# Optimization experiments

Measured on AMD Instinct MI355X. Metric: run time of the kernel, lower is better.

The kernel has to match this reference:

```python
import jax, jax.numpy as jnp
import numpy as np

B, N, U, K = 2, 768, 64, 8
IN = 2 * U + K  # 136
SLOPE = 0.01    # torch LeakyReLU default


def setup_inputs() -> dict:
    key = jax.random.key(0)
    ks = jax.random.split(key, 12)
    seq_embed = jax.random.normal(ks[0], (B, N, U), dtype=jnp.float32)
    vals = jax.random.uniform(ks[1], (N, N, K), dtype=jnp.float32)
    edge = (jax.random.uniform(ks[2], (N, N)) < 0.05) | jnp.eye(N, dtype=bool)
    relational_encoding = vals * edge[:, :, None].astype(jnp.float32)
    s = 0.05
    inp = {"seq_embed": seq_embed, "relational_encoding": relational_encoding}
    # per-hop MLP params: hop k has Linear(IN,IN) then Linear(IN,1); W stored (in,out)
    inp["w1_1"] = jax.random.normal(ks[3], (IN, IN), dtype=jnp.float32) * s
    inp["b1_1"] = jax.random.normal(ks[4], (IN,), dtype=jnp.float32) * s
    inp["w1_2"] = jax.random.normal(ks[5], (IN, 1), dtype=jnp.float32) * s
    inp["b1_2"] = jax.random.normal(ks[6], (1,), dtype=jnp.float32) * s
    inp["w2_1"] = jax.random.normal(ks[7], (IN, IN), dtype=jnp.float32) * s
    inp["b2_1"] = jax.random.normal(ks[8], (IN,), dtype=jnp.float32) * s
    inp["w2_2"] = jax.random.normal(ks[9], (IN, 1), dtype=jnp.float32) * s
    inp["b2_2"] = jax.random.normal(ks[10], (1,), dtype=jnp.float32) * s
    return inp


def _fwd(seq_embed, relational_encoding, hop_params):
    mask = (relational_encoding.sum(-1) > 0).astype(seq_embed.dtype)  # (N,N)
    D = mask.sum(-1)  # (N,) row degree
    rel = relational_encoding[None]  # (1,N,N,K) broadcast over batch
    x = seq_embed
    for layers in hop_params:
        b, n, u = x.shape
        e_i = jnp.broadcast_to(x[:, :, None, :], (b, n, n, u))  # row embed
        e_j = jnp.broadcast_to(x[:, None, :, :], (b, n, n, u))  # col embed
        seq_combined = jnp.concatenate([e_i, e_j], axis=-1)     # (B,N,N,2U)
        combined = jnp.concatenate(
            [seq_combined, jnp.broadcast_to(rel, (b, n, n, rel.shape[-1]))], axis=-1)
        combined = combined * mask[None, :, :, None]
        w = combined
        for (W, bb) in layers:
            w = jax.nn.leaky_relu(w @ W + bb, SLOPE)
        w = w[..., 0] * mask[None]                 # (B,N,N)
        scaled = w / D[None, :, None]              # divide each row i by D[i]
        # weighted neighbor embeds = scaled * e_j, summed over dim 1 (rows)
        x = jnp.einsum('bij,biju->bju', scaled, e_j)
    return x


def reference(seq_embed, relational_encoding, w1_1, b1_1, w1_2, b1_2,
              w2_1, b2_1, w2_2, b2_2):
    hop_params = [[(w1_1, b1_1), (w1_2, b1_2)], [(w2_1, b2_1), (w2_2, b2_2)]]
    return _fwd(seq_embed, relational_encoding, hop_params)
```

## Files before the change

### kernel.cpp

```cpp
#include <hip/hip_runtime.h>

#define NN 768
#define UU 64
#define KK 8
#define INF 136
#define BB 2
#define SLOPE 0.01f
#define RSLOT 80
#define TOTSLOT (NN * RSLOT)

__device__ __forceinline__ float lrelu(float x) { return x > 0.f ? x : SLOPE * x; }


__global__ void k_pairs(const float* __restrict__ rel, int* __restrict__ recs,
                        float* __restrict__ dinv, float* __restrict__ zreg) {
    __shared__ int wcnt[4];
    int i = blockIdx.x;
    int tid = threadIdx.x;
    int w = tid >> 6, lane = tid & 63;

    if (i < 6) {
        zreg[i * 512 + tid] = 0.f;
        zreg[i * 512 + 256 + tid] = 0.f;
    }

    int j0 = w * 192;
    float sums[3];
#pragma unroll
    for (int it = 0; it < 3; it++) {
        int j = j0 + it * 64 + lane;
        const float4* rp = (const float4*)(rel + (size_t)(i * NN + j) * KK);
        float4 a = rp[0], b = rp[1];
        sums[it] = a.x + a.y + a.z + a.w + b.x + b.y + b.z + b.w;
    }
    int cnt = 0;
    int pos[3];
    bool act[3];
#pragma unroll
    for (int it = 0; it < 3; it++) {
        act[it] = sums[it] > 0.f;
        unsigned long long m = __ballot(act[it]);
        pos[it] = cnt + __popcll(m & ((1ull << lane) - 1));
        cnt += __popcll(m);
    }
    if (lane == 0) wcnt[w] = cnt;
    __syncthreads();
    int prefix = 0, total = 0;
#pragma unroll
    for (int ww = 0; ww < 4; ww++) {
        int c = wcnt[ww];
        total += c;
        if (ww < w) prefix += c;
    }
#pragma unroll
    for (int it = 0; it < 3; it++) {
        if (act[it]) {
            int rp = prefix + pos[it];
            if (rp < RSLOT) recs[i * RSLOT + rp] = (i << 16) | (j0 + it * 64 + lane);
        }
    }
    if (tid == 0) dinv[i] = 1.0f / (float)total;
}

__global__ void k_precompute(const float* __restrict__ x, const float* __restrict__ sc,
                             const float* __restrict__ W1,
                             float* __restrict__ A, float* __restrict__ Bv) {
    __shared__ float xs[2][UU];
    int r0 = blockIdx.x * 2;
    int tid = threadIdx.x;
    {
        int rr = tid >> 6, u = tid & 63;
        int bi = r0 + rr;
        float f = sc ? sc[bi] : 1.0f;
        xs[rr][u] = x[(size_t)bi * UU + u] * f;
    }
    __syncthreads();
    for (int m = tid; m < INF; m += 128) {
        float a0 = 0.f, a1 = 0.f, bv0 = 0.f, bv1 = 0.f;
#pragma unroll 8
        for (int u = 0; u < UU; u++) {
            float wa = W1[u * INF + m];
            float wb = W1[(UU + u) * INF + m];
            a0  += xs[0][u] * wa;
            a1  += xs[1][u] * wa;
            bv0 += xs[0][u] * wb;
            bv1 += xs[1][u] * wb;
        }
        A [(size_t) r0      * INF + m] = a0;
        A [(size_t)(r0 + 1) * INF + m] = a1;
        Bv[(size_t) r0      * INF + m] = bv0;
        Bv[(size_t)(r0 + 1) * INF + m] = bv1;
    }
}

__device__ __forceinline__ void process_pair(
        int rec, int lane,
        const float* __restrict__ A, const float* __restrict__ Bv,
        const float* __restrict__ rel, const float* __restrict__ W1R,
        const float* __restrict__ dinv, float* __restrict__ s,
        float b10, float b11, float b12,
        float w20, float w21, float w22, float b2v) {
    if (rec < 0) return;
    int i = rec >> 16, j = rec & 0xffff;
    const float* relp = rel + (size_t)(i * NN + j) * KK;
    float4 ra = ((const float4*)relp)[0];
    float4 rb = ((const float4*)relp)[1];
    float di = dinv[i];
    float rv[8] = {ra.x, ra.y, ra.z, ra.w, rb.x, rb.y, rb.z, rb.w};
    float r0 = b10, r1 = b11, r2 = b12;
#pragma unroll
    for (int k = 0; k < 8; k++) {
        r0 += rv[k] * W1R[k * INF + lane];
        r1 += rv[k] * W1R[k * INF + 64 + lane];
        r2 += rv[k] * W1R[k * INF + 128 + (lane & 7)];
    }
    float dd[BB];
#pragma unroll
    for (int b = 0; b < BB; b++) {
        const float* Ai = A  + ((size_t)b * NN + i) * INF;
        const float* Bj = Bv + ((size_t)b * NN + j) * INF;
        float dot = lrelu(r0 + Ai[lane]      + Bj[lane])      * w20
                  + lrelu(r1 + Ai[64 + lane] + Bj[64 + lane]) * w21;
        if (lane < 8)
            dot += lrelu(r2 + Ai[128 + lane] + Bj[128 + lane]) * w22;
#pragma unroll
        for (int off = 32; off; off >>= 1) dot += __shfl_xor(dot, off, 64);
        dd[b] = dot;
    }
    if (lane == 0)  atomicAdd(&s[j],      lrelu(dd[0] + b2v) * di);
    if (lane == 32) atomicAdd(&s[NN + j], lrelu(dd[1] + b2v) * di);
}

__global__ void __launch_bounds__(256) k_hop(
        const int* __restrict__ recs,
        const float* __restrict__ A, const float* __restrict__ Bv,
        const float* __restrict__ rel, const float* __restrict__ W1,
        const float* __restrict__ b1, const float* __restrict__ w2,
        const float* __restrict__ b2, const float* __restrict__ dinv,
        float* __restrict__ s) {
    int lane = threadIdx.x & 63;
    int wid = (blockIdx.x * blockDim.x + threadIdx.x) >> 6;
    int nw = (gridDim.x * blockDim.x) >> 6;

    float b10 = b1[lane], b11 = b1[64 + lane], b12 = b1[128 + (lane & 7)];
    float w20 = w2[lane], w21 = w2[64 + lane];
    float w22 = (lane < 8) ? w2[128 + lane] : 0.f;
    float b2v = b2[0];
    const float* W1R = W1 + 128 * INF;

    for (int p = wid * 2; p < TOTSLOT; p += nw * 2) {
        int2 r2 = *(const int2*)(recs + p);
        process_pair(r2.x, lane, A, Bv, rel, W1R, dinv, s, b10, b11, b12, w20, w21, w22, b2v);
        process_pair(r2.y, lane, A, Bv, rel, W1R, dinv, s, b10, b11, b12, w20, w21, w22, b2v);
    }
}

__global__ void k_final(const float* __restrict__ seq, const float* __restrict__ s1,
                        const float* __restrict__ s2, float* __restrict__ out) {
    int idx = blockIdx.x * blockDim.x + threadIdx.x;
    if (idx >= BB * NN * UU) return;
    int bj = idx >> 6;
    out[idx] = seq[idx] * s1[bj] * s2[bj];
}

extern "C" void kernel_launch(void* const* d_in, const int* in_sizes, int n_in,
                              void* d_out, int out_size, void* d_ws, size_t ws_size,
                              hipStream_t stream) {
    const float* seq = (const float*)d_in[0];
    const float* rel = (const float*)d_in[1];
    const float* w1_1 = (const float*)d_in[2];
    const float* b1_1 = (const float*)d_in[3];
    const float* w1_2 = (const float*)d_in[4];
    const float* b1_2 = (const float*)d_in[5];
    const float* w2_1 = (const float*)d_in[6];
    const float* b2_1 = (const float*)d_in[7];
    const float* w2_2 = (const float*)d_in[8];
    const float* b2_2 = (const float*)d_in[9];
    float* out = (float*)d_out;

    char* ws = (char*)d_ws;
    float* dinv = (float*)(ws + 0);
    float* s1   = (float*)(ws + 4096);
    float* s2   = (float*)(ws + 10240);
    float* A    = (float*)(ws + 16384);
    float* Bv   = (float*)(ws + 851968);
    int*   recs = (int*)  (ws + 1687552);

    k_pairs<<<NN, 256, 0, stream>>>(rel, recs, dinv, s1);

    k_precompute<<<BB * NN / 2, 128, 0, stream>>>(seq, nullptr, w1_1, A, Bv);
    k_hop<<<1536, 256, 0, stream>>>(recs, A, Bv, rel, w1_1, b1_1, w1_2, b1_2, dinv, s1);

    k_precompute<<<BB * NN / 2, 128, 0, stream>>>(seq, s1, w2_1, A, Bv);
    k_hop<<<1536, 256, 0, stream>>>(recs, A, Bv, rel, w2_1, b2_1, w2_2, b2_2, dinv, s2);

    k_final<<<(BB * NN * UU + 255) / 256, 256, 0, stream>>>(seq, s1, s2, out);
}
```

Measured before the change: 152.7 us.

## Compact pair records globally and fuse pair scan with first precompute

Replaces the fixed 80-slot-per-row record layout with one compacted global list built via an atomic counter, so hop kernels only visit real pairs and skip padded slots. Fuses the pair scan with the first-hop A/B precompute in a single launch, moves zeroing to a memset, and caches W1R rows in registers inside the hop kernel. Each hop thread now handles four records, and the final kernel is vectorized with float4. Records past the 61440-entry cap are silently dropped, and the global atomic makes record order nondeterministic.

```diff
diff --git a/kernel.cpp b/kernel.cpp
--- a/kernel.cpp
+++ b/kernel.cpp
@@ -6,24 +6,61 @@
 #define INF 136
 #define BB 2
 #define SLOPE 0.01f
-#define RSLOT 80
-#define TOTSLOT (NN * RSLOT)
+#define RECCAP 61440
 
 __device__ __forceinline__ float lrelu(float x) { return x > 0.f ? x : SLOPE * x; }
 
 
-__global__ void k_pairs(const float* __restrict__ rel, int* __restrict__ recs,
-                        float* __restrict__ dinv, float* __restrict__ zreg) {
+__device__ __forceinline__ void pre_rows(int r4base, const float* __restrict__ x,
+                                         const float* __restrict__ sc,
+                                         const float* __restrict__ W1,
+                                         float* __restrict__ A, float* __restrict__ Bv,
+                                         float (*xs)[UU], int tid) {
+    {
+        int rr = tid >> 6, u = tid & 63;
+        int bi = r4base + rr;
+        float f = sc ? sc[bi] : 1.0f;
+        xs[rr][u] = x[(size_t)bi * UU + u] * f;
+    }
+    __syncthreads();
+    int m = tid;
+    if (m < INF) {
+        float a[4] = {0.f, 0.f, 0.f, 0.f}, bv[4] = {0.f, 0.f, 0.f, 0.f};
+        for (int u = 0; u < UU; u++) {
+            float wa = W1[u * INF + m];
+            float wb = W1[(UU + u) * INF + m];
+#pragma unroll
+            for (int r = 0; r < 4; r++) {
+                a[r]  += xs[r][u] * wa;
+                bv[r] += xs[r][u] * wb;
+            }
+        }
+#pragma unroll
+        for (int r = 0; r < 4; r++) {
+            A [(size_t)(r4base + r) * INF + m] = a[r];
+            Bv[(size_t)(r4base + r) * INF + m] = bv[r];
+        }
+    }
+}
+
+__global__ void __launch_bounds__(256) k_fused0(
+        const float* __restrict__ rel, const float* __restrict__ seq,
+        const float* __restrict__ W1, int* __restrict__ recs,
+        float* __restrict__ dinv, int* __restrict__ gcount,
+        float* __restrict__ A, float* __restrict__ Bv) {
+    __shared__ float xs[4][UU];
     __shared__ int wcnt[4];
-    int i = blockIdx.x;
+    __shared__ int sbase;
+    int blk = blockIdx.x;
     int tid = threadIdx.x;
+
+    if (blk >= NN) {
+        pre_rows((blk - NN) * 4, seq, nullptr, W1, A, Bv, xs, tid);
+        return;
+    }
+
+    int i = blk;
     int w = tid >> 6, lane = tid & 63;
-
-    if (i < 6) {
-        zreg[i * 512 + tid] = 0.f;
-        zreg[i * 512 + 256 + tid] = 0.f;
-    }
-
     int j0 = w * 192;
     float sums[3];
 #pragma unroll
@@ -52,87 +89,31 @@
         total += c;
         if (ww < w) prefix += c;
     }
+    if (tid == 0) {
+        sbase = atomicAdd(gcount, total);
+        dinv[i] = 1.0f / (float)total;
+    }
+    __syncthreads();
+    int base = sbase;
 #pragma unroll
     for (int it = 0; it < 3; it++) {
         if (act[it]) {
-            int rp = prefix + pos[it];
-            if (rp < RSLOT) recs[i * RSLOT + rp] = (i << 16) | (j0 + it * 64 + lane);
-        }
-    }
-    if (tid == 0) dinv[i] = 1.0f / (float)total;
-}
-
-__global__ void k_precompute(const float* __restrict__ x, const float* __restrict__ sc,
-                             const float* __restrict__ W1,
-                             float* __restrict__ A, float* __restrict__ Bv) {
-    __shared__ float xs[2][UU];
-    int r0 = blockIdx.x * 2;
-    int tid = threadIdx.x;
-    {
-        int rr = tid >> 6, u = tid & 63;
-        int bi = r0 + rr;
-        float f = sc ? sc[bi] : 1.0f;
-        xs[rr][u] = x[(size_t)bi * UU + u] * f;
-    }
-    __syncthreads();
-    for (int m = tid; m < INF; m += 128) {
-        float a0 = 0.f, a1 = 0.f, bv0 = 0.f, bv1 = 0.f;
-#pragma unroll 8
-        for (int u = 0; u < UU; u++) {
-            float wa = W1[u * INF + m];
-            float wb = W1[(UU + u) * INF + m];
-            a0  += xs[0][u] * wa;
-            a1  += xs[1][u] * wa;
-            bv0 += xs[0][u] * wb;
-            bv1 += xs[1][u] * wb;
-        }
-        A [(size_t) r0      * INF + m] = a0;
-        A [(size_t)(r0 + 1) * INF + m] = a1;
-        Bv[(size_t) r0      * INF + m] = bv0;
-        Bv[(size_t)(r0 + 1) * INF + m] = bv1;
-    }
-}
-
-__device__ __forceinline__ void process_pair(
-        int rec, int lane,
-        const float* __restrict__ A, const float* __restrict__ Bv,
-        const float* __restrict__ rel, const float* __restrict__ W1R,
-        const float* __restrict__ dinv, float* __restrict__ s,
-        float b10, float b11, float b12,
-        float w20, float w21, float w22, float b2v) {
-    if (rec < 0) return;
-    int i = rec >> 16, j = rec & 0xffff;
-    const float* relp = rel + (size_t)(i * NN + j) * KK;
-    float4 ra = ((const float4*)relp)[0];
-    float4 rb = ((const float4*)relp)[1];
-    float di = dinv[i];
-    float rv[8] = {ra.x, ra.y, ra.z, ra.w, rb.x, rb.y, rb.z, rb.w};
-    float r0 = b10, r1 = b11, r2 = b12;
-#pragma unroll
-    for (int k = 0; k < 8; k++) {
-        r0 += rv[k] * W1R[k * INF + lane];
-        r1 += rv[k] * W1R[k * INF + 64 + lane];
-        r2 += rv[k] * W1R[k * INF + 128 + (lane & 7)];
-    }
-    float dd[BB];
-#pragma unroll
-    for (int b = 0; b < BB; b++) {
-        const float* Ai = A  + ((size_t)b * NN + i) * INF;
-        const float* Bj = Bv + ((size_t)b * NN + j) * INF;
-        float dot = lrelu(r0 + Ai[lane]      + Bj[lane])      * w20
-                  + lrelu(r1 + Ai[64 + lane] + Bj[64 + lane]) * w21;
-        if (lane < 8)
-            dot += lrelu(r2 + Ai[128 + lane] + Bj[128 + lane]) * w22;
-#pragma unroll
-        for (int off = 32; off; off >>= 1) dot += __shfl_xor(dot, off, 64);
-        dd[b] = dot;
-    }
-    if (lane == 0)  atomicAdd(&s[j],      lrelu(dd[0] + b2v) * di);
-    if (lane == 32) atomicAdd(&s[NN + j], lrelu(dd[1] + b2v) * di);
+            int rp = base + prefix + pos[it];
+            if (rp < RECCAP) recs[rp] = (i << 16) | (j0 + it * 64 + lane);
+        }
+    }
+}
+
+__global__ void __launch_bounds__(256) k_pre(const float* __restrict__ x,
+                                             const float* __restrict__ sc,
+                                             const float* __restrict__ W1,
+                                             float* __restrict__ A, float* __restrict__ Bv) {
+    __shared__ float xs[4][UU];
+    pre_rows(blockIdx.x * 4, x, sc, W1, A, Bv, xs, threadIdx.x);
 }
 
 __global__ void __launch_bounds__(256) k_hop(
-        const int* __restrict__ recs,
+        const int* __restrict__ recs, const int* __restrict__ gcount,
         const float* __restrict__ A, const float* __restrict__ Bv,
         const float* __restrict__ rel, const float* __restrict__ W1,
         const float* __restrict__ b1, const float* __restrict__ w2,
@@ -140,27 +121,71 @@
         float* __restrict__ s) {
     int lane = threadIdx.x & 63;
     int wid = (blockIdx.x * blockDim.x + threadIdx.x) >> 6;
-    int nw = (gridDim.x * blockDim.x) >> 6;
-
+    int cnt = *gcount;
+    int p = wid * 4;
+    if (p >= cnt) return;
+
+    const float* W1R = W1 + 128 * INF;
+    float w1r0[8], w1r1[8], w1r2[8];
+#pragma unroll
+    for (int k = 0; k < 8; k++) {
+        w1r0[k] = W1R[k * INF + lane];
+        w1r1[k] = W1R[k * INF + 64 + lane];
+        w1r2[k] = W1R[k * INF + 128 + (lane & 7)];
+    }
     float b10 = b1[lane], b11 = b1[64 + lane], b12 = b1[128 + (lane & 7)];
     float w20 = w2[lane], w21 = w2[64 + lane];
     float w22 = (lane < 8) ? w2[128 + lane] : 0.f;
     float b2v = b2[0];
-    const float* W1R = W1 + 128 * INF;
-
-    for (int p = wid * 2; p < TOTSLOT; p += nw * 2) {
-        int2 r2 = *(const int2*)(recs + p);
-        process_pair(r2.x, lane, A, Bv, rel, W1R, dinv, s, b10, b11, b12, w20, w21, w22, b2v);
-        process_pair(r2.y, lane, A, Bv, rel, W1R, dinv, s, b10, b11, b12, w20, w21, w22, b2v);
-    }
-}
-
-__global__ void k_final(const float* __restrict__ seq, const float* __restrict__ s1,
-                        const float* __restrict__ s2, float* __restrict__ out) {
+
+    int4 q = *(const int4*)(recs + p);
+    int rr4[4] = {q.x, q.y, q.z, q.w};
+
+#pragma unroll
+    for (int t = 0; t < 4; t++) {
+        if (p + t >= cnt) break;
+        int rec = rr4[t];
+        int i = rec >> 16, j = rec & 0xffff;
+        const float* relp = rel + (size_t)(i * NN + j) * KK;
+        float4 ra = ((const float4*)relp)[0];
+        float4 rb = ((const float4*)relp)[1];
+        float di = dinv[i];
+        float rv[8] = {ra.x, ra.y, ra.z, ra.w, rb.x, rb.y, rb.z, rb.w};
+        float r0 = b10, r1 = b11, r2 = b12;
+#pragma unroll
+        for (int k = 0; k < 8; k++) {
+            r0 += rv[k] * w1r0[k];
+            r1 += rv[k] * w1r1[k];
+            r2 += rv[k] * w1r2[k];
+        }
+        float dd[BB];
+#pragma unroll
+        for (int b = 0; b < BB; b++) {
+            const float* Ai = A  + ((size_t)b * NN + i) * INF;
+            const float* Bj = Bv + ((size_t)b * NN + j) * INF;
+            float dot = lrelu(r0 + Ai[lane]      + Bj[lane])      * w20
+                      + lrelu(r1 + Ai[64 + lane] + Bj[64 + lane]) * w21;
+            if (lane < 8)
+                dot += lrelu(r2 + Ai[128 + lane] + Bj[128 + lane]) * w22;
+#pragma unroll
+            for (int off = 32; off; off >>= 1) dot += __shfl_xor(dot, off, 64);
+            dd[b] = dot;
+        }
+        if (lane == 0)  atomicAdd(&s[j],      lrelu(dd[0] + b2v) * di);
+        if (lane == 32) atomicAdd(&s[NN + j], lrelu(dd[1] + b2v) * di);
+    }
+}
+
+__global__ void __launch_bounds__(256) k_final(const float4* __restrict__ seq,
+                                               const float* __restrict__ s1,
+                                               const float* __restrict__ s2,
+                                               float4* __restrict__ out) {
     int idx = blockIdx.x * blockDim.x + threadIdx.x;
-    if (idx >= BB * NN * UU) return;
-    int bj = idx >> 6;
-    out[idx] = seq[idx] * s1[bj] * s2[bj];
+    int bj = idx >> 4;
+    float f = s1[bj] * s2[bj];
+    float4 v = seq[idx];
+    v.x *= f; v.y *= f; v.z *= f; v.w *= f;
+    out[idx] = v;
 }
 
 extern "C" void kernel_launch(void* const* d_in, const int* in_sizes, int n_in,
@@ -179,20 +204,22 @@
     float* out = (float*)d_out;
 
     char* ws = (char*)d_ws;
-    float* dinv = (float*)(ws + 0);
-    float* s1   = (float*)(ws + 4096);
-    float* s2   = (float*)(ws + 10240);
-    float* A    = (float*)(ws + 16384);
-    float* Bv   = (float*)(ws + 851968);
-    int*   recs = (int*)  (ws + 1687552);
-
-    k_pairs<<<NN, 256, 0, stream>>>(rel, recs, dinv, s1);
-
-    k_precompute<<<BB * NN / 2, 128, 0, stream>>>(seq, nullptr, w1_1, A, Bv);
-    k_hop<<<1536, 256, 0, stream>>>(recs, A, Bv, rel, w1_1, b1_1, w1_2, b1_2, dinv, s1);
-
-    k_precompute<<<BB * NN / 2, 128, 0, stream>>>(seq, s1, w2_1, A, Bv);
-    k_hop<<<1536, 256, 0, stream>>>(recs, A, Bv, rel, w2_1, b2_1, w2_2, b2_2, dinv, s2);
-
-    k_final<<<(BB * NN * UU + 255) / 256, 256, 0, stream>>>(seq, s1, s2, out);
-}
+    float* s1     = (float*)(ws + 0);
+    float* s2     = (float*)(ws + 6144);
+    int*   gcount = (int*)  (ws + 12288);
+    float* dinv   = (float*)(ws + 12544);
+    float* A      = (float*)(ws + 16384);
+    float* Bv     = (float*)(ws + 851968);
+    int*   recs   = (int*)  (ws + 1687552);
+
+    hipMemsetAsync(ws, 0, 12292, stream);
+
+    k_fused0<<<NN + 384, 256, 0, stream>>>(rel, seq, w1_1, recs, dinv, gcount, A, Bv);
+
+    k_hop<<<RECCAP / 16, 256, 0, stream>>>(recs, gcount, A, Bv, rel, w1_1, b1_1, w1_2, b1_2, dinv, s1);
+
+    k_pre<<<384, 256, 0, stream>>>(seq, s1, w2_1, A, Bv);
+    k_hop<<<RECCAP / 16, 256, 0, stream>>>(recs, gcount, A, Bv, rel, w2_1, b2_1, w2_2, b2_2, dinv, s2);
+
+    k_final<<<BB * NN * UU / 4 / 256, 256, 0, stream>>>((const float4*)seq, s1, s2, (float4*)out);
+}
```

After: 155.4 us. Within noise of the previous version (+1.7%).
